# Optimization experiments

Hardware: AMD Instinct MI355X
Metric: run time of the kernel (lower is better)

## Reference

```python
import jax, jax.numpy as jnp
import numpy as np

N = 50000      # nodes
E = 800000     # edges
IN = 256       # in_dim
D = 64         # hidden_dim per head
H = 4          # heads
OUT = 40       # out_dim (classes)
SLOPE = 0.2    # leaky relu negative slope


def _gat_conv(h, src, dst, W, al, ar, heads, dh, res=None, act=False):
    """DGL-style GATConv. h:[N,Fin], W:[Fin,heads*dh], al/ar:[heads,dh]."""
    n = h.shape[0]
    feat = (h @ W).reshape(n, heads, dh)                 # [N,H,D]
    el = jnp.sum(feat * al, axis=-1)                     # [N,H]
    er = jnp.sum(feat * ar, axis=-1)                     # [N,H]
    e = jax.nn.leaky_relu(el[src] + er[dst], SLOPE)      # [E,H]
    # segment softmax over incoming edges of each dst node
    m = jax.ops.segment_max(e, dst, num_segments=n)      # [N,H]
    ex = jnp.exp(e - m[dst])                             # [E,H]
    s = jax.ops.segment_sum(ex, dst, num_segments=n)     # [N,H]
    alpha = ex / s[dst]                                  # [E,H]
    rst = jax.ops.segment_sum(alpha[:, :, None] * feat[src], dst, num_segments=n)  # [N,H,D]
    if res is not None:
        rst = rst + res
    if act:
        rst = jax.nn.elu(rst)
    return rst


def setup_inputs():
    key = jax.random.key(0)
    ks = jax.random.split(key, 16)
    def p(k, shape, fan_in):
        return (jax.random.normal(k, shape, jnp.float32) / np.sqrt(fan_in)).astype(jnp.float32)
    inputs = jax.random.normal(ks[0], (N, IN), jnp.float32)
    src = jax.random.randint(ks[1], (E,), 0, N, dtype=jnp.int32)
    dst = jax.random.randint(ks[2], (E,), 0, N, dtype=jnp.int32)
    return {
        "inputs": inputs, "src": src, "dst": dst,
        "W0": p(ks[3], (IN, H * D), IN), "al0": p(ks[4], (H, D), D), "ar0": p(ks[5], (H, D), D),
        "W1": p(ks[6], (H * D, H * D), H * D), "al1": p(ks[7], (H, D), D), "ar1": p(ks[8], (H, D), D),
        "Wo": p(ks[9], (H * D, H * OUT), H * D), "alo": p(ks[10], (H, OUT), OUT), "aro": p(ks[11], (H, OUT), OUT),
        "res_Wo": p(ks[12], (H * D, H * OUT), H * D),
        "fc_W": p(ks[13], (IN, D), IN),
    }


def reference(inputs, src, dst, W0, al0, ar0, W1, al1, ar1, Wo, alo, aro, res_Wo, fc_W):
    # layer 0: no residual, elu activation
    h = _gat_conv(inputs, src, dst, W0, al0, ar0, H, D, res=None, act=True)
    h = h.reshape(N, H * D)
    # layer 1: identity residual (in_feats == heads*out_feats), elu
    res1 = h.reshape(N, H, D)
    h = _gat_conv(h, src, dst, W1, al1, ar1, H, D, res=res1, act=True)
    h = h.reshape(N, H * D)
    # output layer: linear residual projection, no activation, mean over heads
    res_o = (h @ res_Wo).reshape(N, H, OUT)
    logits = _gat_conv(h, src, dst, Wo, alo, aro, H, OUT, res=res_o, act=False).mean(axis=1)
    seq_fts = inputs @ fc_W
    return (logits, h, seq_fts)
```

## Files before the change

### kernel.cpp

```cpp
#include <hip/hip_runtime.h>

typedef unsigned short u16;
typedef unsigned int u32;
typedef __attribute__((ext_vector_type(8))) short short8;
typedef __attribute__((ext_vector_type(4))) float f32x4;

#define NN 50000
#define EE 800000
#define EPAD (EE + 8*NN)

__device__ __forceinline__ float b2f(u16 u){ union{float f;u32 i;}x; x.i=((u32)u)<<16; return x.f; }
__device__ __forceinline__ u16 f2b(float f){ union{float f;u32 i;}x; x.f=f; u32 i=x.i; return (u16)((i + 0x7fffu + ((i>>16)&1u))>>16); }

__global__ void k_f2b4(const float* __restrict__ x, u16* __restrict__ y, int n4){
  int i = blockIdx.x*256 + threadIdx.x;
  if (i >= n4) return;
  float4 v = ((const float4*)x)[i];
  ushort4 o; o.x=f2b(v.x); o.y=f2b(v.y); o.z=f2b(v.z); o.w=f2b(v.w);
  ((ushort4*)y)[i]=o;
}

__global__ void k_wtr(const float* __restrict__ W, u16* __restrict__ Wt, int N){
  int i = blockIdx.x*256 + threadIdx.x;
  if (i >= 256*N) return;
  int k = i / N, n = i % N;
  Wt[(size_t)n*256 + k] = f2b(W[i]);
}

__global__ void k_catWoT(const float* __restrict__ rWo, const float* __restrict__ Wo, u16* __restrict__ Bct){
  int i = blockIdx.x*256 + threadIdx.x;
  if (i >= 256*320) return;
  int k = i/320, c = i%320;
  float v = (c < 160) ? rWo[k*160 + c] : Wo[k*160 + (c-160)];
  Bct[(size_t)c*256 + k] = f2b(v);
}

__global__ void k_count(const int* __restrict__ dst, int* __restrict__ cnt){
  int i = blockIdx.x*256+threadIdx.x; if (i<EE) atomicAdd(&cnt[dst[i]],1);
}

__global__ void k_scan_blocks(const int* __restrict__ cnt, int* __restrict__ off, int* __restrict__ part, int n){
  __shared__ int ts[256];
  int t = threadIdx.x; int base = blockIdx.x*1024 + t*4;
  int c0 = (base+0<n)?((cnt[base+0]+7)&~7):0;
  int c1 = (base+1<n)?((cnt[base+1]+7)&~7):0;
  int c2 = (base+2<n)?((cnt[base+2]+7)&~7):0;
  int c3 = (base+3<n)?((cnt[base+3]+7)&~7):0;
  int s = c0+c1+c2+c3;
  ts[t]=s; __syncthreads();
  for (int d=1; d<256; d<<=1){ int v=(t>=d)?ts[t-d]:0; __syncthreads(); ts[t]+=v; __syncthreads(); }
  int ex = ts[t]-s;
  if (t==255) part[blockIdx.x]=ts[255];
  if (base+0<n) off[base+0]=ex; ex+=c0;
  if (base+1<n) off[base+1]=ex; ex+=c1;
  if (base+2<n) off[base+2]=ex; ex+=c2;
  if (base+3<n) off[base+3]=ex;
}

__global__ void k_scan_part(int* part, int nb){
  if (threadIdx.x==0 && blockIdx.x==0){ int run=0; for(int i=0;i<nb;++i){ int v=part[i]; part[i]=run; run+=v; } }
}

__global__ void k_addback(int* off, int* cur, const int* __restrict__ part, int n){
  int base = blockIdx.x*1024 + threadIdx.x*4; int p = part[blockIdx.x];
  #pragma unroll
  for (int j=0;j<4;++j) if (base+j<n){ int v = off[base+j]+p; off[base+j]=v; if (base+j<NN) cur[base+j]=v; }
}

__global__ void k_scatter(const int* __restrict__ src, const int* __restrict__ dst, int* __restrict__ cur,
                          int* __restrict__ srcs){
  int i = blockIdx.x*256+threadIdx.x; if (i>=EE) return;
  int d = dst[i]; int p = atomicAdd(&cur[d],1);
  srcs[p]=src[i];
}

template<int BN, int MODE>
__global__ __launch_bounds__(256) void k_gemm2(const u16* __restrict__ A, const u16* __restrict__ Bt,
                                               void* __restrict__ C0, void* __restrict__ C1,
                                               int M, int ldC){
  __shared__ u16 lds[(128+BN)*256];
  u16* As = lds;
  u16* Bs = lds + 128*256;
  const int tid = threadIdx.x;
  const int row0 = blockIdx.x * 128;
  const int n0   = blockIdx.y * BN;
  #pragma unroll
  for (int it=0; it<16; ++it){
    int slot = it*256 + tid;
    int r = slot >> 5, s = slot & 31;
    int gs = s ^ (r & 7);
    const u16* gp = A + (size_t)(row0 + r)*256 + (gs<<3);
    u16* lp = As + (size_t)(it*256 + (tid & ~63))*8;
    __builtin_amdgcn_global_load_lds((const void*)gp, (void*)lp, 16, 0, 0);
  }
  #pragma unroll
  for (int it=0; it<BN/8; ++it){
    int slot = it*256 + tid;
    int r = slot >> 5, s = slot & 31;
    int gs = s ^ (r & 7);
    const u16* gp = Bt + (size_t)(n0 + r)*256 + (gs<<3);
    u16* lp = Bs + (size_t)(it*256 + (tid & ~63))*8;
    __builtin_amdgcn_global_load_lds((const void*)gp, (void*)lp, 16, 0, 0);
  }
  __syncthreads();
  const int wave = tid >> 6, l = tid & 63;
  const int wm = wave >> 1, wn = wave & 1;
  const int lr = l & 15, lq = l >> 4;
  const int NR = BN/32;
  f32x4 acc[4][4];
  #pragma unroll
  for (int mr=0;mr<4;++mr)
    #pragma unroll
    for (int nr=0;nr<NR;++nr) acc[mr][nr]=(f32x4)0.0f;
  #pragma unroll
  for (int kk=0; kk<8; ++kk){
    short8 a[4], b[4];
    #pragma unroll
    for (int mr=0;mr<4;++mr){
      int rloc = wm*64 + mr*16 + lr;
      int byo = rloc*512 + ((kk*64 + lq*16) ^ ((rloc&7)<<4));
      a[mr] = *(const short8*)((const char*)As + byo);
    }
    #pragma unroll
    for (int nr=0;nr<NR;++nr){
      int cloc = wn*(BN/2) + nr*16 + lr;
      int byo = cloc*512 + ((kk*64 + lq*16) ^ ((cloc&7)<<4));
      b[nr] = *(const short8*)((const char*)Bs + byo);
    }
    #pragma unroll
    for (int mr=0;mr<4;++mr)
      #pragma unroll
      for (int nr=0;nr<NR;++nr)
        acc[mr][nr] = __builtin_amdgcn_mfma_f32_16x16x32_bf16(a[mr], b[nr], acc[mr][nr], 0, 0, 0);
  }
  #pragma unroll
  for (int mr=0;mr<4;++mr)
    #pragma unroll
    for (int nr=0;nr<NR;++nr)
      #pragma unroll
      for (int q=0;q<4;++q){
        int r = row0 + wm*64 + mr*16 + lq*4 + q;
        if (r < M){
          int c = n0 + wn*(BN/2) + nr*16 + lr;
          float v = acc[mr][nr][q];
          if constexpr (MODE == 0)      ((float*)C0)[(size_t)r*ldC + c] = v;
          else if constexpr (MODE == 1) ((u16*)C0)[(size_t)r*ldC + c] = f2b(v);
          else {
            if (c < 160)      ((u16*)C0)[(size_t)r*160 + c]       = f2b(v);
            else if (c < 320) ((u16*)C1)[(size_t)r*160 + (c-160)] = f2b(v);
          }
        }
      }
}

__global__ void k_eler256(const u16* __restrict__ feat, const float* __restrict__ al, const float* __restrict__ ar,
                          float* __restrict__ el, float* __restrict__ er){
  int t = blockIdx.x*256 + threadIdx.x;
  int n = t >> 6, l = t & 63;
  if (n >= NN) return;
  float4 a4 = ((const float4*)al)[l];
  float4 r4 = ((const float4*)ar)[l];
  ushort4 f = *(const ushort4*)(feat + (size_t)n*256 + l*4);
  float f0=b2f(f.x), f1=b2f(f.y), f2=b2f(f.z), f3=b2f(f.w);
  float accl = f0*a4.x + f1*a4.y + f2*a4.z + f3*a4.w;
  float accr = f0*r4.x + f1*r4.y + f2*r4.z + f3*r4.w;
  #pragma unroll
  for (int m = 8; m >= 1; m >>= 1){ accl += __shfl_xor(accl, m, 64); accr += __shfl_xor(accr, m, 64); }
  int h = l >> 4;
  if ((l & 15) == 0){ el[n*4+h] = accl; er[n*4+h] = accr; }
}

__global__ void k_eler(const u16* __restrict__ feat, const float* __restrict__ al, const float* __restrict__ ar,
                       float* __restrict__ el, float* __restrict__ er, int Dh, int HD){
  int t = blockIdx.x*256 + threadIdx.x;
  int n = t >> 6; int l = t & 63;
  if (n >= NN) return;
  int h = l >> 4, s = l & 15;
  const u16* fr = feat + (size_t)n*HD + h*Dh;
  const float* alh = al + h*Dh; const float* arh = ar + h*Dh;
  float accl = 0.f, accr = 0.f;
  for (int d = s; d < Dh; d += 16){ float f = b2f(fr[d]); accl += f*alh[d]; accr += f*arh[d]; }
  #pragma unroll
  for (int m = 8; m >= 1; m >>= 1){ accl += __shfl_xor(accl, m, 64); accr += __shfl_xor(accr, m, 64); }
  if (s == 0){ el[n*4+h] = accl; er[n*4+h] = accr; }
}

__global__ void k_soft(const float* __restrict__ el, const float* __restrict__ er,
                       const int* __restrict__ srcs, const int* __restrict__ off, const int* __restrict__ cnt,
                       float* __restrict__ es, float* __restrict__ recs){
  int t = blockIdx.x*256 + threadIdx.x;
  int n = t >> 4; if (n >= NN) return;
  int g = t & 15;
  int o0 = off[n], o1p = off[n+1];
  int deg = cnt[n];
  int oend = o0 + deg;
  float4 e4 = ((const float4*)er)[n];
  float4 m; m.x=m.y=m.z=m.w=-1e30f;
  for (int c = o0 + g; c < oend; c += 16){
    float4 a = ((const float4*)el)[srcs[c]];
    float4 v;
    v.x=a.x+e4.x; v.x = v.x>=0.f?v.x:0.2f*v.x;
    v.y=a.y+e4.y; v.y = v.y>=0.f?v.y:0.2f*v.y;
    v.z=a.z+e4.z; v.z = v.z>=0.f?v.z:0.2f*v.z;
    v.w=a.w+e4.w; v.w = v.w>=0.f?v.w:0.2f*v.w;
    ((float4*)es)[c]=v;
    m.x=fmaxf(m.x,v.x); m.y=fmaxf(m.y,v.y); m.z=fmaxf(m.z,v.z); m.w=fmaxf(m.w,v.w);
  }
  { int cp = oend + g; if (cp < o1p){ float4 z; z.x=z.y=z.z=z.w=0.f; ((float4*)es)[cp]=z; } }
  #pragma unroll
  for (int msk = 8; msk >= 1; msk >>= 1){
    m.x=fmaxf(m.x,__shfl_xor(m.x,msk,64)); m.y=fmaxf(m.y,__shfl_xor(m.y,msk,64));
    m.z=fmaxf(m.z,__shfl_xor(m.z,msk,64)); m.w=fmaxf(m.w,__shfl_xor(m.w,msk,64));
  }
  float4 s; s.x=s.y=s.z=s.w=0.f;
  for (int c = o0 + g; c < oend; c += 16){
    float4 v = ((const float4*)es)[c];
    v.x=__expf(v.x-m.x); v.y=__expf(v.y-m.y); v.z=__expf(v.z-m.z); v.w=__expf(v.w-m.w);
    ((float4*)es)[c]=v; s.x+=v.x; s.y+=v.y; s.z+=v.z; s.w+=v.w;
  }
  #pragma unroll
  for (int msk = 8; msk >= 1; msk >>= 1){
    s.x+=__shfl_xor(s.x,msk,64); s.y+=__shfl_xor(s.y,msk,64);
    s.z+=__shfl_xor(s.z,msk,64); s.w+=__shfl_xor(s.w,msk,64);
  }
  if (g == 0){
    float4 r;
    r.x = s.x>0.f ? 1.f/s.x : 0.f;
    r.y = s.y>0.f ? 1.f/s.y : 0.f;
    r.z = s.z>0.f ? 1.f/s.z : 0.f;
    r.w = s.w>0.f ? 1.f/s.w : 0.f;
    ((float4*)recs)[n] = r;
  }
}

template<bool RES>
__global__ __launch_bounds__(256) void k_agg64(const u16* __restrict__ feat, const float* __restrict__ es,
    const float* __restrict__ recs, const int* __restrict__ off, const int* __restrict__ srcs,
    const u16* __restrict__ resid, float* __restrict__ outf, u16* __restrict__ outb){
  const int l = threadIdx.x & 63, w = threadIdx.x >> 6;
  const int n = blockIdx.x*4 + w;
  const int o0 = off[n], o1p = off[n+1];
  const int lh = l & 31;
  const int half = l >> 5;
  const int h = lh >> 3;
  float a0=0.f,a1=0.f,a2=0.f,a3=0.f,a4=0.f,a5=0.f,a6=0.f,a7=0.f;
  int i = o0;
  for (; i + 16 <= o1p; i += 16){
    #pragma unroll
    for (int u=0; u<8; ++u){
      int e = i + u*2 + half;
      int sv = srcs[e];
      float al = es[(size_t)e*4 + h];
      short8 f = *(const short8*)(feat + (size_t)sv*256 + lh*8);
      a0 += al*b2f((u16)f[0]); a1 += al*b2f((u16)f[1]);
      a2 += al*b2f((u16)f[2]); a3 += al*b2f((u16)f[3]);
      a4 += al*b2f((u16)f[4]); a5 += al*b2f((u16)f[5]);
      a6 += al*b2f((u16)f[6]); a7 += al*b2f((u16)f[7]);
    }
  }
  if (i < o1p){
    #pragma unroll
    for (int u=0; u<4; ++u){
      int e = i + u*2 + half;
      int sv = srcs[e];
      float al = es[(size_t)e*4 + h];
      short8 f = *(const short8*)(feat + (size_t)sv*256 + lh*8);
      a0 += al*b2f((u16)f[0]); a1 += al*b2f((u16)f[1]);
      a2 += al*b2f((u16)f[2]); a3 += al*b2f((u16)f[3]);
      a4 += al*b2f((u16)f[4]); a5 += al*b2f((u16)f[5]);
      a6 += al*b2f((u16)f[6]); a7 += al*b2f((u16)f[7]);
    }
  }
  a0 += __shfl_xor(a0,32,64); a1 += __shfl_xor(a1,32,64);
  a2 += __shfl_xor(a2,32,64); a3 += __shfl_xor(a3,32,64);
  a4 += __shfl_xor(a4,32,64); a5 += __shfl_xor(a5,32,64);
  a6 += __shfl_xor(a6,32,64); a7 += __shfl_xor(a7,32,64);
  if (half == 0){
    float rc = recs[n*4+h];
    float v[8] = {a0*rc,a1*rc,a2*rc,a3*rc,a4*rc,a5*rc,a6*rc,a7*rc};
    if (RES){
      short8 r8 = *(const short8*)(resid + (size_t)n*256 + lh*8);
      #pragma unroll
      for (int j=0;j<8;++j) v[j] += b2f((u16)r8[j]);
    }
    #pragma unroll
    for (int j=0;j<8;++j) v[j] = v[j] > 0.f ? v[j] : expm1f(v[j]);
    if (outf){
      float4 q0; q0.x=v[0]; q0.y=v[1]; q0.z=v[2]; q0.w=v[3];
      float4 q1; q1.x=v[4]; q1.y=v[5]; q1.z=v[6]; q1.w=v[7];
      *(float4*)(outf + (size_t)n*256 + lh*8)     = q0;
      *(float4*)(outf + (size_t)n*256 + lh*8 + 4) = q1;
    }
    short8 ob;
    #pragma unroll
    for (int j=0;j<8;++j) ob[j] = (short)f2b(v[j]);
    *(short8*)(outb + (size_t)n*256 + lh*8) = ob;
  }
}

__global__ __launch_bounds__(256) void k_agg_out(const u16* __restrict__ feat, const float* __restrict__ es,
    const float* __restrict__ recs, const int* __restrict__ off, const int* __restrict__ srcs,
    const u16* __restrict__ reso, float* __restrict__ logits){
  __shared__ float red[4][8][20][8];
  __shared__ float fin[4][160];
  const int l = threadIdx.x & 63, w = threadIdx.x >> 6;
  const int n = blockIdx.x*4 + w;
  const int o0 = off[n], o1p = off[n+1];
  const int s0 = l/20,        q0 = l%20;
  const int s1 = (64+l)/20,   q1 = (64+l)%20;
  const int s2 = (128+l)/20,  q2 = (128+l)%20;
  const int h0 = q0/5, h1 = q1/5, h2 = q2/5;
  float acc0[8], acc1[8], acc2[8];
  #pragma unroll
  for (int j=0;j<8;++j){ acc0[j]=0.f; acc1[j]=0.f; acc2[j]=0.f; }
  for (int i0 = o0; i0 < o1p; i0 += 8){
    {
      int e = i0 + s0; int sv = srcs[e]; float al = es[(size_t)e*4 + h0];
      short8 f = *(const short8*)(feat + (size_t)sv*160 + q0*8);
      #pragma unroll
      for (int j=0;j<8;++j) acc0[j] += al*b2f((u16)f[j]);
    }
    {
      int e = i0 + s1; int sv = srcs[e]; float al = es[(size_t)e*4 + h1];
      short8 f = *(const short8*)(feat + (size_t)sv*160 + q1*8);
      #pragma unroll
      for (int j=0;j<8;++j) acc1[j] += al*b2f((u16)f[j]);
    }
    if (l < 32){
      int e = i0 + s2; int sv = srcs[e]; float al = es[(size_t)e*4 + h2];
      short8 f = *(const short8*)(feat + (size_t)sv*160 + q2*8);
      #pragma unroll
      for (int j=0;j<8;++j) acc2[j] += al*b2f((u16)f[j]);
    }
  }
  #pragma unroll
  for (int j=0;j<8;++j) red[w][s0][q0][j] = acc0[j];
  #pragma unroll
  for (int j=0;j<8;++j) red[w][s1][q1][j] = acc1[j];
  if (l < 32){
    #pragma unroll
    for (int j=0;j<8;++j) red[w][s2][q2][j] = acc2[j];
  }
  __syncthreads();
  if (l < 20){
    const int q = l;
    float rc = recs[n*4 + q/5];
    short8 rr = *(const short8*)(reso + (size_t)n*160 + q*8);
    #pragma unroll
    for (int j=0;j<8;++j){
      float v = red[w][0][q][j];
      #pragma unroll
      for (int s=1;s<8;++s) v += red[w][s][q][j];
      fin[w][q*8+j] = v*rc + b2f((u16)rr[j]);
    }
  }
  __syncthreads();
  if (l < 40) logits[(size_t)n*40 + l] = 0.25f*(fin[w][l]+fin[w][l+40]+fin[w][l+80]+fin[w][l+120]);
}

extern "C" void kernel_launch(void* const* d_in, const int* in_sizes, int n_in,
                              void* d_out, int out_size, void* d_ws, size_t ws_size,
                              hipStream_t stream){
  const float* inputs = (const float*)d_in[0];
  const int*   src    = (const int*)d_in[1];
  const int*   dst    = (const int*)d_in[2];
  const float* W0  = (const float*)d_in[3];
  const float* al0 = (const float*)d_in[4];
  const float* ar0 = (const float*)d_in[5];
  const float* W1  = (const float*)d_in[6];
  const float* al1 = (const float*)d_in[7];
  const float* ar1 = (const float*)d_in[8];
  const float* Wo  = (const float*)d_in[9];
  const float* alo = (const float*)d_in[10];
  const float* aro = (const float*)d_in[11];
  const float* rWo = (const float*)d_in[12];
  const float* fcW = (const float*)d_in[13];

  float* out = (float*)d_out;
  float* out_logits = out;
  float* out_h      = out + 2000000;
  float* out_seq    = out + 14800000;

  char* ws = (char*)d_ws;
  size_t o = 0;
  auto alc = [&](size_t bytes){ size_t r = o; o += (bytes + 255) & ~(size_t)255; return r; };
  size_t oXb   = alc((size_t)NN*256*2);
  size_t oFA   = alc((size_t)NN*256*2);
  size_t oFB   = alc((size_t)NN*256*2);
  size_t oEs   = alc((size_t)EPAD*4*4);
  size_t oSrcs = alc((size_t)EPAD*4);
  size_t oOff  = alc((size_t)(NN+1)*4);
  size_t oCnt  = alc((size_t)(NN+1)*4);
  size_t oCur  = alc((size_t)NN*4);
  size_t oPart = alc(64*4);
  size_t oEl   = alc((size_t)NN*4*4);
  size_t oEr   = alc((size_t)NN*4*4);
  size_t oRecs = alc((size_t)NN*4*4);
  size_t oReso = alc((size_t)NN*160*2);
  size_t oW0t  = alc(256*256*2);
  size_t oW1t  = alc(256*256*2);
  size_t oWct  = alc((size_t)384*256*2);
  size_t oFct  = alc((size_t)128*256*2);
  if (ws_size < o) return;

  u16* Xb   = (u16*)(ws + oXb);
  u16* fA   = (u16*)(ws + oFA);
  u16* fB   = (u16*)(ws + oFB);
  float* es = (float*)(ws + oEs);
  int* srcs = (int*)(ws + oSrcs);
  int* off  = (int*)(ws + oOff);
  int* cnt  = (int*)(ws + oCnt);
  int* cur  = (int*)(ws + oCur);
  int* part = (int*)(ws + oPart);
  float* el = (float*)(ws + oEl);
  float* er = (float*)(ws + oEr);
  float* recs = (float*)(ws + oRecs);
  u16* reso = (u16*)(ws + oReso);
  u16* W0t  = (u16*)(ws + oW0t);
  u16* W1t  = (u16*)(ws + oW1t);
  u16* Wct  = (u16*)(ws + oWct);
  u16* fct  = (u16*)(ws + oFct);

  k_f2b4<<<(NN*256/4 + 255)/256, 256, 0, stream>>>(inputs, Xb, NN*256/4);
  k_wtr<<<(256*256 + 255)/256, 256, 0, stream>>>(W0, W0t, 256);
  k_wtr<<<(256*256 + 255)/256, 256, 0, stream>>>(W1, W1t, 256);
  k_wtr<<<(256*64 + 255)/256, 256, 0, stream>>>(fcW, fct, 64);
  k_catWoT<<<(256*320 + 255)/256, 256, 0, stream>>>(rWo, Wo, Wct);

  hipMemsetAsync(cnt, 0, (size_t)(NN+1)*4, stream);
  hipMemsetAsync(srcs, 0, (size_t)EPAD*4, stream);
  k_count<<<(EE+255)/256, 256, 0, stream>>>(dst, cnt);
  const int NP1 = NN+1, NB = (NP1 + 1023)/1024;
  k_scan_blocks<<<NB, 256, 0, stream>>>(cnt, off, part, NP1);
  k_scan_part<<<1, 64, 0, stream>>>(part, NB);
  k_addback<<<NB, 256, 0, stream>>>(off, cur, part, NP1);
  k_scatter<<<(EE+255)/256, 256, 0, stream>>>(src, dst, cur, srcs);

  const int GX = (NN + 127)/128;
  dim3 g256(GX, 2), g320(GX, 3), g64(GX, 1);

  k_gemm2<64,0><<<g64, 256, 0, stream>>>(Xb, fct, out_seq, nullptr, NN, 64);

  k_gemm2<128,1><<<g256, 256, 0, stream>>>(Xb, W0t, fA, nullptr, NN, 256);
  k_eler256<<<(NN*64 + 255)/256, 256, 0, stream>>>(fA, al0, ar0, el, er);
  k_soft<<<(NN*16 + 255)/256, 256, 0, stream>>>(el, er, srcs, off, cnt, es, recs);
  k_agg64<false><<<NN/4, 256, 0, stream>>>(fA, es, recs, off, srcs, nullptr, nullptr, fB);

  k_gemm2<128,1><<<g256, 256, 0, stream>>>(fB, W1t, fA, nullptr, NN, 256);
  k_eler256<<<(NN*64 + 255)/256, 256, 0, stream>>>(fA, al1, ar1, el, er);
  k_soft<<<(NN*16 + 255)/256, 256, 0, stream>>>(el, er, srcs, off, cnt, es, recs);
  k_agg64<true><<<NN/4, 256, 0, stream>>>(fA, es, recs, off, srcs, fB, out_h, fB);

  k_gemm2<128,2><<<g320, 256, 0, stream>>>(fB, Wct, reso, fA, NN, 320);
  k_eler<<<(NN*64 + 255)/256, 256, 0, stream>>>(fA, alo, aro, el, er, 40, 160);
  k_soft<<<(NN*16 + 255)/256, 256, 0, stream>>>(el, er, srcs, off, cnt, es, recs);
  k_agg_out<<<NN/4, 256, 0, stream>>>(fA, es, recs, off, srcs, reso, out_logits);
}
```

Measured before the change: 489.7 us.

## Fuse attention logits into GEMM epilogue and softmax into aggregation kernels

The el/er attention dot products for the two 256-wide layers are now computed in the GEMM epilogue from the fp32 accumulators using lane shuffles, which removes the separate k_eler256 launch and its re-read of the feature matrix. The segment softmax (max, exp, sum) moves into the aggregation kernels: each wave handles one destination node, and padded edge slots are written as -1e30 so they contribute zero after the exp. This drops three k_soft launches and the recs buffer. In exchange, the aggregation loop loses its 16-edge unrolled main loop and now steps 8 edges at a time. The epilogue reduction also uses the rounded-before-bf16 fp32 values, so el/er differ slightly from before.

```diff
diff --git a/kernel.cpp b/kernel.cpp
--- a/kernel.cpp
+++ b/kernel.cpp
@@ -77,6 +77,8 @@
 template<int BN, int MODE>
 __global__ __launch_bounds__(256) void k_gemm2(const u16* __restrict__ A, const u16* __restrict__ Bt,
                                                void* __restrict__ C0, void* __restrict__ C1,
+                                               const float* __restrict__ AL, const float* __restrict__ AR,
+                                               float* __restrict__ EL, float* __restrict__ ER,
                                                int M, int ldC){
   __shared__ u16 lds[(128+BN)*256];
   u16* As = lds;
@@ -151,23 +153,26 @@
           }
         }
       }
-}
-
-__global__ void k_eler256(const u16* __restrict__ feat, const float* __restrict__ al, const float* __restrict__ ar,
-                          float* __restrict__ el, float* __restrict__ er){
-  int t = blockIdx.x*256 + threadIdx.x;
-  int n = t >> 6, l = t & 63;
-  if (n >= NN) return;
-  float4 a4 = ((const float4*)al)[l];
-  float4 r4 = ((const float4*)ar)[l];
-  ushort4 f = *(const ushort4*)(feat + (size_t)n*256 + l*4);
-  float f0=b2f(f.x), f1=b2f(f.y), f2=b2f(f.z), f3=b2f(f.w);
-  float accl = f0*a4.x + f1*a4.y + f2*a4.z + f3*a4.w;
-  float accr = f0*r4.x + f1*r4.y + f2*r4.z + f3*r4.w;
-  #pragma unroll
-  for (int m = 8; m >= 1; m >>= 1){ accl += __shfl_xor(accl, m, 64); accr += __shfl_xor(accr, m, 64); }
-  int h = l >> 4;
-  if ((l & 15) == 0){ el[n*4+h] = accl; er[n*4+h] = accr; }
+  if constexpr (MODE == 1){
+    const int head = (n0 + wn*64) >> 6;
+    float alc[4], arc[4];
+    #pragma unroll
+    for (int nr=0;nr<4;++nr){
+      int c = n0 + wn*64 + nr*16 + lr;
+      alc[nr] = AL[c]; arc[nr] = AR[c];
+    }
+    #pragma unroll
+    for (int mr=0;mr<4;++mr)
+      #pragma unroll
+      for (int q=0;q<4;++q){
+        float suml = acc[mr][0][q]*alc[0] + acc[mr][1][q]*alc[1] + acc[mr][2][q]*alc[2] + acc[mr][3][q]*alc[3];
+        float sumr = acc[mr][0][q]*arc[0] + acc[mr][1][q]*arc[1] + acc[mr][2][q]*arc[2] + acc[mr][3][q]*arc[3];
+        #pragma unroll
+        for (int msk=1; msk<16; msk<<=1){ suml += __shfl_xor(suml,msk,64); sumr += __shfl_xor(sumr,msk,64); }
+        int r = row0 + wm*64 + mr*16 + lq*4 + q;
+        if (lr == 0 && r < M){ EL[r*4+head] = suml; ER[r*4+head] = sumr; }
+      }
+  }
 }
 
 __global__ void k_eler(const u16* __restrict__ feat, const float* __restrict__ al, const float* __restrict__ ar,
@@ -185,80 +190,63 @@
   if (s == 0){ el[n*4+h] = accl; er[n*4+h] = accr; }
 }
 
-__global__ void k_soft(const float* __restrict__ el, const float* __restrict__ er,
-                       const int* __restrict__ srcs, const int* __restrict__ off, const int* __restrict__ cnt,
-                       float* __restrict__ es, float* __restrict__ recs){
-  int t = blockIdx.x*256 + threadIdx.x;
-  int n = t >> 4; if (n >= NN) return;
-  int g = t & 15;
-  int o0 = off[n], o1p = off[n+1];
-  int deg = cnt[n];
-  int oend = o0 + deg;
-  float4 e4 = ((const float4*)er)[n];
+__device__ __forceinline__ float4 soft_prefix(const float* __restrict__ el, float4 e4,
+    const int* __restrict__ srcs, float* __restrict__ es, int o0, int o1p, int oend, int l){
   float4 m; m.x=m.y=m.z=m.w=-1e30f;
-  for (int c = o0 + g; c < oend; c += 16){
-    float4 a = ((const float4*)el)[srcs[c]];
+  for (int e = o0 + l; e < o1p; e += 64){
     float4 v;
-    v.x=a.x+e4.x; v.x = v.x>=0.f?v.x:0.2f*v.x;
-    v.y=a.y+e4.y; v.y = v.y>=0.f?v.y:0.2f*v.y;
-    v.z=a.z+e4.z; v.z = v.z>=0.f?v.z:0.2f*v.z;
-    v.w=a.w+e4.w; v.w = v.w>=0.f?v.w:0.2f*v.w;
-    ((float4*)es)[c]=v;
+    if (e < oend){
+      float4 a = ((const float4*)el)[srcs[e]];
+      v.x=a.x+e4.x; v.x=v.x>=0.f?v.x:0.2f*v.x;
+      v.y=a.y+e4.y; v.y=v.y>=0.f?v.y:0.2f*v.y;
+      v.z=a.z+e4.z; v.z=v.z>=0.f?v.z:0.2f*v.z;
+      v.w=a.w+e4.w; v.w=v.w>=0.f?v.w:0.2f*v.w;
+    } else { v.x=v.y=v.z=v.w=-1e30f; }
+    ((float4*)es)[e] = v;
     m.x=fmaxf(m.x,v.x); m.y=fmaxf(m.y,v.y); m.z=fmaxf(m.z,v.z); m.w=fmaxf(m.w,v.w);
   }
-  { int cp = oend + g; if (cp < o1p){ float4 z; z.x=z.y=z.z=z.w=0.f; ((float4*)es)[cp]=z; } }
-  #pragma unroll
-  for (int msk = 8; msk >= 1; msk >>= 1){
+  #pragma unroll
+  for (int msk=1; msk<64; msk<<=1){
     m.x=fmaxf(m.x,__shfl_xor(m.x,msk,64)); m.y=fmaxf(m.y,__shfl_xor(m.y,msk,64));
     m.z=fmaxf(m.z,__shfl_xor(m.z,msk,64)); m.w=fmaxf(m.w,__shfl_xor(m.w,msk,64));
   }
   float4 s; s.x=s.y=s.z=s.w=0.f;
-  for (int c = o0 + g; c < oend; c += 16){
-    float4 v = ((const float4*)es)[c];
+  for (int e = o0 + l; e < o1p; e += 64){
+    float4 v = ((const float4*)es)[e];
     v.x=__expf(v.x-m.x); v.y=__expf(v.y-m.y); v.z=__expf(v.z-m.z); v.w=__expf(v.w-m.w);
-    ((float4*)es)[c]=v; s.x+=v.x; s.y+=v.y; s.z+=v.z; s.w+=v.w;
-  }
-  #pragma unroll
-  for (int msk = 8; msk >= 1; msk >>= 1){
+    ((float4*)es)[e]=v;
+    s.x+=v.x; s.y+=v.y; s.z+=v.z; s.w+=v.w;
+  }
+  #pragma unroll
+  for (int msk=1; msk<64; msk<<=1){
     s.x+=__shfl_xor(s.x,msk,64); s.y+=__shfl_xor(s.y,msk,64);
     s.z+=__shfl_xor(s.z,msk,64); s.w+=__shfl_xor(s.w,msk,64);
   }
-  if (g == 0){
-    float4 r;
-    r.x = s.x>0.f ? 1.f/s.x : 0.f;
-    r.y = s.y>0.f ? 1.f/s.y : 0.f;
-    r.z = s.z>0.f ? 1.f/s.z : 0.f;
-    r.w = s.w>0.f ? 1.f/s.w : 0.f;
-    ((float4*)recs)[n] = r;
-  }
+  float4 rc;
+  rc.x = s.x>0.f ? 1.f/s.x : 0.f;
+  rc.y = s.y>0.f ? 1.f/s.y : 0.f;
+  rc.z = s.z>0.f ? 1.f/s.z : 0.f;
+  rc.w = s.w>0.f ? 1.f/s.w : 0.f;
+  return rc;
 }
 
 template<bool RES>
-__global__ __launch_bounds__(256) void k_agg64(const u16* __restrict__ feat, const float* __restrict__ es,
-    const float* __restrict__ recs, const int* __restrict__ off, const int* __restrict__ srcs,
+__global__ __launch_bounds__(256) void k_agg64(const u16* __restrict__ feat,
+    const float* __restrict__ el, const float* __restrict__ er, float* __restrict__ es,
+    const int* __restrict__ off, const int* __restrict__ cnt, const int* __restrict__ srcs,
     const u16* __restrict__ resid, float* __restrict__ outf, u16* __restrict__ outb){
   const int l = threadIdx.x & 63, w = threadIdx.x >> 6;
   const int n = blockIdx.x*4 + w;
   const int o0 = off[n], o1p = off[n+1];
+  const int oend = o0 + cnt[n];
+  float4 e4 = ((const float4*)er)[n];
+  float4 rc4 = soft_prefix(el, e4, srcs, es, o0, o1p, oend, l);
   const int lh = l & 31;
   const int half = l >> 5;
   const int h = lh >> 3;
+  const float rch = ((const float*)&rc4)[h];
   float a0=0.f,a1=0.f,a2=0.f,a3=0.f,a4=0.f,a5=0.f,a6=0.f,a7=0.f;
-  int i = o0;
-  for (; i + 16 <= o1p; i += 16){
-    #pragma unroll
-    for (int u=0; u<8; ++u){
-      int e = i + u*2 + half;
-      int sv = srcs[e];
-      float al = es[(size_t)e*4 + h];
-      short8 f = *(const short8*)(feat + (size_t)sv*256 + lh*8);
-      a0 += al*b2f((u16)f[0]); a1 += al*b2f((u16)f[1]);
-      a2 += al*b2f((u16)f[2]); a3 += al*b2f((u16)f[3]);
-      a4 += al*b2f((u16)f[4]); a5 += al*b2f((u16)f[5]);
-      a6 += al*b2f((u16)f[6]); a7 += al*b2f((u16)f[7]);
-    }
-  }
-  if (i < o1p){
+  for (int i = o0; i < o1p; i += 8){
     #pragma unroll
     for (int u=0; u<4; ++u){
       int e = i + u*2 + half;
@@ -276,8 +264,7 @@
   a4 += __shfl_xor(a4,32,64); a5 += __shfl_xor(a5,32,64);
   a6 += __shfl_xor(a6,32,64); a7 += __shfl_xor(a7,32,64);
   if (half == 0){
-    float rc = recs[n*4+h];
-    float v[8] = {a0*rc,a1*rc,a2*rc,a3*rc,a4*rc,a5*rc,a6*rc,a7*rc};
+    float v[8] = {a0*rch,a1*rch,a2*rch,a3*rch,a4*rch,a5*rch,a6*rch,a7*rch};
     if (RES){
       short8 r8 = *(const short8*)(resid + (size_t)n*256 + lh*8);
       #pragma unroll
@@ -298,14 +285,18 @@
   }
 }
 
-__global__ __launch_bounds__(256) void k_agg_out(const u16* __restrict__ feat, const float* __restrict__ es,
-    const float* __restrict__ recs, const int* __restrict__ off, const int* __restrict__ srcs,
+__global__ __launch_bounds__(256) void k_agg_out(const u16* __restrict__ feat,
+    const float* __restrict__ el, const float* __restrict__ er, float* __restrict__ es,
+    const int* __restrict__ off, const int* __restrict__ cnt, const int* __restrict__ srcs,
     const u16* __restrict__ reso, float* __restrict__ logits){
   __shared__ float red[4][8][20][8];
   __shared__ float fin[4][160];
   const int l = threadIdx.x & 63, w = threadIdx.x >> 6;
   const int n = blockIdx.x*4 + w;
   const int o0 = off[n], o1p = off[n+1];
+  const int oend = o0 + cnt[n];
+  float4 e4 = ((const float4*)er)[n];
+  float4 rc4 = soft_prefix(el, e4, srcs, es, o0, o1p, oend, l);
   const int s0 = l/20,        q0 = l%20;
   const int s1 = (64+l)/20,   q1 = (64+l)%20;
   const int s2 = (128+l)/20,  q2 = (128+l)%20;
@@ -344,7 +335,7 @@
   __syncthreads();
   if (l < 20){
     const int q = l;
-    float rc = recs[n*4 + q/5];
+    float rc = ((const float*)&rc4)[q/5];
     short8 rr = *(const short8*)(reso + (size_t)n*160 + q*8);
     #pragma unroll
     for (int j=0;j<8;++j){
@@ -395,7 +386,6 @@
   size_t oPart = alc(64*4);
   size_t oEl   = alc((size_t)NN*4*4);
   size_t oEr   = alc((size_t)NN*4*4);
-  size_t oRecs = alc((size_t)NN*4*4);
   size_t oReso = alc((size_t)NN*160*2);
   size_t oW0t  = alc(256*256*2);
   size_t oW1t  = alc(256*256*2);
@@ -414,7 +404,6 @@
   int* part = (int*)(ws + oPart);
   float* el = (float*)(ws + oEl);
   float* er = (float*)(ws + oEr);
-  float* recs = (float*)(ws + oRecs);
   u16* reso = (u16*)(ws + oReso);
   u16* W0t  = (u16*)(ws + oW0t);
   u16* W1t  = (u16*)(ws + oW1t);
@@ -439,20 +428,15 @@
   const int GX = (NN + 127)/128;
   dim3 g256(GX, 2), g320(GX, 3), g64(GX, 1);
 
-  k_gemm2<64,0><<<g64, 256, 0, stream>>>(Xb, fct, out_seq, nullptr, NN, 64);
-
-  k_gemm2<128,1><<<g256, 256, 0, stream>>>(Xb, W0t, fA, nullptr, NN, 256);
-  k_eler256<<<(NN*64 + 255)/256, 256, 0, stream>>>(fA, al0, ar0, el, er);
-  k_soft<<<(NN*16 + 255)/256, 256, 0, stream>>>(el, er, srcs, off, cnt, es, recs);
-  k_agg64<false><<<NN/4, 256, 0, stream>>>(fA, es, recs, off, srcs, nullptr, nullptr, fB);
-
-  k_gemm2<128,1><<<g256, 256, 0, stream>>>(fB, W1t, fA, nullptr, NN, 256);
-  k_eler256<<<(NN*64 + 255)/256, 256, 0, stream>>>(fA, al1, ar1, el, er);
-  k_soft<<<(NN*16 + 255)/256, 256, 0, stream>>>(el, er, srcs, off, cnt, es, recs);
-  k_agg64<true><<<NN/4, 256, 0, stream>>>(fA, es, recs, off, srcs, fB, out_h, fB);
-
-  k_gemm2<128,2><<<g320, 256, 0, stream>>>(fB, Wct, reso, fA, NN, 320);
+  k_gemm2<64,0><<<g64, 256, 0, stream>>>(Xb, fct, out_seq, nullptr, nullptr, nullptr, nullptr, nullptr, NN, 64);
+
+  k_gemm2<128,1><<<g256, 256, 0, stream>>>(Xb, W0t, fA, nullptr, al0, ar0, el, er, NN, 256);
+  k_agg64<false><<<NN/4, 256, 0, stream>>>(fA, el, er, es, off, cnt, srcs, nullptr, nullptr, fB);
+
+  k_gemm2<128,1><<<g256, 256, 0, stream>>>(fB, W1t, fA, nullptr, al1, ar1, el, er, NN, 256);
+  k_agg64<true><<<NN/4, 256, 0, stream>>>(fA, el, er, es, off, cnt, srcs, fB, out_h, fB);
+
+  k_gemm2<128,2><<<g320, 256, 0, stream>>>(fB, Wct, reso, fA, nullptr, nullptr, nullptr, nullptr, NN, 320);
   k_eler<<<(NN*64 + 255)/256, 256, 0, stream>>>(fA, alo, aro, el, er, 40, 160);
-  k_soft<<<(NN*16 + 255)/256, 256, 0, stream>>>(el, er, srcs, off, cnt, es, recs);
-  k_agg_out<<<NN/4, 256, 0, stream>>>(fA, es, recs, off, srcs, reso, out_logits);
-}
+  k_agg_out<<<NN/4, 256, 0, stream>>>(fA, el, er, es, off, cnt, srcs, reso, out_logits);
+}
```

New measurement: 512.6 us. 4.7% more time.

## Fuse attention logit dot products into GEMM epilogue and trim padding memset

Applied to the files above, without the earlier changes.

The per-head el/er dot products for the two hidden GAT layers are now computed in the MODE 1 GEMM epilogue from fp32 accumulators, using shuffle reductions, which removes two k_eler256 launches and their re-reads of the bf16 features. The full memset of the padded source-index array is replaced by a kernel that zeroes only the padding slots after each node's edges. The aggregation loop is simplified to a single 8-edge stride, and an LDS reduction array in the output aggregation is padded to avoid bank conflicts. The logits now come from unrounded fp32 values rather than bf16 features, which changes numerics slightly and adds register pressure and shuffles to the GEMM epilogue.

```diff
diff --git a/kernel.cpp b/kernel.cpp
--- a/kernel.cpp
+++ b/kernel.cpp
@@ -74,9 +74,17 @@
   srcs[p]=src[i];
 }
 
+__global__ void k_padfill(const int* __restrict__ off, const int* __restrict__ cnt, int* __restrict__ srcs){
+  int n = blockIdx.x*256+threadIdx.x; if (n>=NN) return;
+  int e = off[n]+cnt[n], e1 = off[n+1];
+  for (; e<e1; ++e) srcs[e] = 0;
+}
+
 template<int BN, int MODE>
 __global__ __launch_bounds__(256) void k_gemm2(const u16* __restrict__ A, const u16* __restrict__ Bt,
                                                void* __restrict__ C0, void* __restrict__ C1,
+                                               const float* __restrict__ AL, const float* __restrict__ AR,
+                                               float* __restrict__ EL, float* __restrict__ ER,
                                                int M, int ldC){
   __shared__ u16 lds[(128+BN)*256];
   u16* As = lds;
@@ -151,23 +159,26 @@
           }
         }
       }
-}
-
-__global__ void k_eler256(const u16* __restrict__ feat, const float* __restrict__ al, const float* __restrict__ ar,
-                          float* __restrict__ el, float* __restrict__ er){
-  int t = blockIdx.x*256 + threadIdx.x;
-  int n = t >> 6, l = t & 63;
-  if (n >= NN) return;
-  float4 a4 = ((const float4*)al)[l];
-  float4 r4 = ((const float4*)ar)[l];
-  ushort4 f = *(const ushort4*)(feat + (size_t)n*256 + l*4);
-  float f0=b2f(f.x), f1=b2f(f.y), f2=b2f(f.z), f3=b2f(f.w);
-  float accl = f0*a4.x + f1*a4.y + f2*a4.z + f3*a4.w;
-  float accr = f0*r4.x + f1*r4.y + f2*r4.z + f3*r4.w;
-  #pragma unroll
-  for (int m = 8; m >= 1; m >>= 1){ accl += __shfl_xor(accl, m, 64); accr += __shfl_xor(accr, m, 64); }
-  int h = l >> 4;
-  if ((l & 15) == 0){ el[n*4+h] = accl; er[n*4+h] = accr; }
+  if constexpr (MODE == 1){
+    const int head = (n0 + wn*64) >> 6;
+    float alc[4], arc[4];
+    #pragma unroll
+    for (int nr=0;nr<4;++nr){
+      int c = n0 + wn*64 + nr*16 + lr;
+      alc[nr] = AL[c]; arc[nr] = AR[c];
+    }
+    #pragma unroll
+    for (int mr=0;mr<4;++mr)
+      #pragma unroll
+      for (int q=0;q<4;++q){
+        float suml = acc[mr][0][q]*alc[0] + acc[mr][1][q]*alc[1] + acc[mr][2][q]*alc[2] + acc[mr][3][q]*alc[3];
+        float sumr = acc[mr][0][q]*arc[0] + acc[mr][1][q]*arc[1] + acc[mr][2][q]*arc[2] + acc[mr][3][q]*arc[3];
+        #pragma unroll
+        for (int msk=1; msk<16; msk<<=1){ suml += __shfl_xor(suml,msk,64); sumr += __shfl_xor(sumr,msk,64); }
+        int r = row0 + wm*64 + mr*16 + lq*4 + q;
+        if (lr == 0 && r < M){ EL[r*4+head] = suml; ER[r*4+head] = sumr; }
+      }
+  }
 }
 
 __global__ void k_eler(const u16* __restrict__ feat, const float* __restrict__ al, const float* __restrict__ ar,
@@ -244,21 +255,7 @@
   const int half = l >> 5;
   const int h = lh >> 3;
   float a0=0.f,a1=0.f,a2=0.f,a3=0.f,a4=0.f,a5=0.f,a6=0.f,a7=0.f;
-  int i = o0;
-  for (; i + 16 <= o1p; i += 16){
-    #pragma unroll
-    for (int u=0; u<8; ++u){
-      int e = i + u*2 + half;
-      int sv = srcs[e];
-      float al = es[(size_t)e*4 + h];
-      short8 f = *(const short8*)(feat + (size_t)sv*256 + lh*8);
-      a0 += al*b2f((u16)f[0]); a1 += al*b2f((u16)f[1]);
-      a2 += al*b2f((u16)f[2]); a3 += al*b2f((u16)f[3]);
-      a4 += al*b2f((u16)f[4]); a5 += al*b2f((u16)f[5]);
-      a6 += al*b2f((u16)f[6]); a7 += al*b2f((u16)f[7]);
-    }
-  }
-  if (i < o1p){
+  for (int i = o0; i < o1p; i += 8){
     #pragma unroll
     for (int u=0; u<4; ++u){
       int e = i + u*2 + half;
@@ -301,7 +298,7 @@
 __global__ __launch_bounds__(256) void k_agg_out(const u16* __restrict__ feat, const float* __restrict__ es,
     const float* __restrict__ recs, const int* __restrict__ off, const int* __restrict__ srcs,
     const u16* __restrict__ reso, float* __restrict__ logits){
-  __shared__ float red[4][8][20][8];
+  __shared__ float red[4][8][20][9];
   __shared__ float fin[4][160];
   const int l = threadIdx.x & 63, w = threadIdx.x >> 6;
   const int n = blockIdx.x*4 + w;
@@ -428,30 +425,28 @@
   k_catWoT<<<(256*320 + 255)/256, 256, 0, stream>>>(rWo, Wo, Wct);
 
   hipMemsetAsync(cnt, 0, (size_t)(NN+1)*4, stream);
-  hipMemsetAsync(srcs, 0, (size_t)EPAD*4, stream);
   k_count<<<(EE+255)/256, 256, 0, stream>>>(dst, cnt);
   const int NP1 = NN+1, NB = (NP1 + 1023)/1024;
   k_scan_blocks<<<NB, 256, 0, stream>>>(cnt, off, part, NP1);
   k_scan_part<<<1, 64, 0, stream>>>(part, NB);
   k_addback<<<NB, 256, 0, stream>>>(off, cur, part, NP1);
   k_scatter<<<(EE+255)/256, 256, 0, stream>>>(src, dst, cur, srcs);
+  k_padfill<<<(NN+255)/256, 256, 0, stream>>>(off, cnt, srcs);
 
   const int GX = (NN + 127)/128;
   dim3 g256(GX, 2), g320(GX, 3), g64(GX, 1);
 
-  k_gemm2<64,0><<<g64, 256, 0, stream>>>(Xb, fct, out_seq, nullptr, NN, 64);
-
-  k_gemm2<128,1><<<g256, 256, 0, stream>>>(Xb, W0t, fA, nullptr, NN, 256);
-  k_eler256<<<(NN*64 + 255)/256, 256, 0, stream>>>(fA, al0, ar0, el, er);
+  k_gemm2<64,0><<<g64, 256, 0, stream>>>(Xb, fct, out_seq, nullptr, nullptr, nullptr, nullptr, nullptr, NN, 64);
+
+  k_gemm2<128,1><<<g256, 256, 0, stream>>>(Xb, W0t, fA, nullptr, al0, ar0, el, er, NN, 256);
   k_soft<<<(NN*16 + 255)/256, 256, 0, stream>>>(el, er, srcs, off, cnt, es, recs);
   k_agg64<false><<<NN/4, 256, 0, stream>>>(fA, es, recs, off, srcs, nullptr, nullptr, fB);
 
-  k_gemm2<128,1><<<g256, 256, 0, stream>>>(fB, W1t, fA, nullptr, NN, 256);
-  k_eler256<<<(NN*64 + 255)/256, 256, 0, stream>>>(fA, al1, ar1, el, er);
+  k_gemm2<128,1><<<g256, 256, 0, stream>>>(fB, W1t, fA, nullptr, al1, ar1, el, er, NN, 256);
   k_soft<<<(NN*16 + 255)/256, 256, 0, stream>>>(el, er, srcs, off, cnt, es, recs);
   k_agg64<true><<<NN/4, 256, 0, stream>>>(fA, es, recs, off, srcs, fB, out_h, fB);
 
-  k_gemm2<128,2><<<g320, 256, 0, stream>>>(fB, Wct, reso, fA, NN, 320);
+  k_gemm2<128,2><<<g320, 256, 0, stream>>>(fB, Wct, reso, fA, nullptr, nullptr, nullptr, nullptr, NN, 320);
   k_eler<<<(NN*64 + 255)/256, 256, 0, stream>>>(fA, alo, aro, el, er, 40, 160);
   k_soft<<<(NN*16 + 255)/256, 256, 0, stream>>>(el, er, srcs, off, cnt, es, recs);
   k_agg_out<<<NN/4, 256, 0, stream>>>(fA, es, recs, off, srcs, reso, out_logits);
```

Result: no change. 492.4 us (+0.6%).
